# Kernel tuning notes

Measured on AMD Instinct MI355X. Metric: run time of the kernel, lower is better.

Reference implementation:

```python
import jax, jax.numpy as jnp
import numpy as np

B, C, S = 16, 8, 128
DT, DX, DY = 0.001, 1.0, 1.0
NUM_STEPS = 10
EPS = 1e-6


def _thomas(a, b, c, d):
    """Batched Thomas tridiagonal solve. a,b,c,d: [M,N] rows; solve along N."""
    aT, bT, cT, dT = a.T, b.T, c.T, d.T  # [N, M]
    zero = jnp.zeros_like(dT[0])

    def fwd(carry, inp):
        cs_p, ds_p = carry
        ai, bi, ci, di = inp
        denom = bi - ai * cs_p + EPS  # i=0: cs_p=0 -> denom = b0 + eps (matches torch)
        cs = ci / denom
        ds = (di - ai * ds_p) / denom
        return (cs, ds), (cs, ds)

    _, (c_star, d_star) = jax.lax.scan(fwd, (zero, zero), (aT, bT, cT, dT))

    def bwd(x_next, inp):
        ci, di = inp
        x = di - ci * x_next
        return x, x

    _, xs = jax.lax.scan(bwd, d_star[-1], (c_star[:-1], d_star[:-1]), reverse=True)
    x = jnp.concatenate([xs, d_star[-1:]], axis=0)  # [N, M]
    return x.T


def _diffuse_rows(u2d, coeff):
    """Implicit 1D diffusion along last axis. u2d, coeff: [M,N]."""
    a = -coeff
    c = -coeff
    b = 1.0 + 2.0 * coeff
    b = b.at[:, 0].set(1.0 + coeff[:, 0])
    b = b.at[:, -1].set(1.0 + coeff[:, -1])
    return _thomas(a, b, c, u2d)


def _forward(u, alpha_base, beta_base, alpha_time_coeff, beta_time_coeff, channel_mixing):
    Bb, Cc, H, W = u.shape
    half = DT / 2.0
    t = 0.0
    for _ in range(NUM_STEPS):
        # x half-step (coefficient alpha at time t)
        alpha = jnp.clip(alpha_base + alpha_time_coeff * t, EPS, 10.0)
        u = jnp.einsum('dc,bchw->bdhw', channel_mixing, u)
        uf = u.reshape(Bb * Cc, H, W)
        af = jnp.broadcast_to(alpha[None], (Bb, Cc, H, W)).reshape(Bb * Cc, H, W)
        uf = _diffuse_rows(uf.reshape(-1, W), af.reshape(-1, W) * half / DX**2).reshape(Bb * Cc, H, W)
        t += half
        # y full step (coefficient beta at time t+dt/2)
        beta = jnp.clip(beta_base + beta_time_coeff * t, EPS, 10.0)
        bf = jnp.broadcast_to(beta[None], (Bb, Cc, H, W)).reshape(Bb * Cc, H, W)
        ut = uf.transpose(0, 2, 1).reshape(-1, H)
        bt = bf.transpose(0, 2, 1).reshape(-1, H)
        ut = _diffuse_rows(ut, bt * DT / DY**2)
        uf = ut.reshape(Bb * Cc, W, H).transpose(0, 2, 1)
        t += half
        # x half-step (coefficient alpha at time t+dt)
        alpha = jnp.clip(alpha_base + alpha_time_coeff * t, EPS, 10.0)
        af = jnp.broadcast_to(alpha[None], (Bb, Cc, H, W)).reshape(Bb * Cc, H, W)
        uf = _diffuse_rows(uf.reshape(-1, W), af.reshape(-1, W) * half / DX**2).reshape(Bb * Cc, H, W)
        u = uf.reshape(Bb, Cc, H, W)
    return u


def setup_inputs() -> dict:
    key = jax.random.key(0)
    k_u, k_cm, k_atc, k_btc = jax.random.split(key, 4)
    u = jax.random.normal(k_u, (B, C, S, S), dtype=jnp.float32)
    alpha_base = jnp.ones((C, S, S), dtype=jnp.float32)
    beta_base = jnp.ones((C, S, S), dtype=jnp.float32)
    alpha_time_coeff = jax.random.normal(k_atc, (C, S, S), dtype=jnp.float32) * 0.01
    beta_time_coeff = jax.random.normal(k_btc, (C, S, S), dtype=jnp.float32) * 0.01
    channel_mixing = jnp.eye(C, dtype=jnp.float32) + jax.random.normal(k_cm, (C, C), dtype=jnp.float32) * 0.01
    return {
        'u': u,
        'alpha_base': alpha_base,
        'beta_base': beta_base,
        'alpha_time_coeff': alpha_time_coeff,
        'beta_time_coeff': beta_time_coeff,
        'channel_mixing': channel_mixing,
    }


def reference(u, alpha_base, beta_base, alpha_time_coeff, beta_time_coeff, channel_mixing):
    return _forward(u, alpha_base, beta_base, alpha_time_coeff, beta_time_coeff, channel_mixing)
```

## Files before the change

### kernel.cpp

```cpp
#include <hip/hip_runtime.h>
#include <hip/hip_fp16.h>


constexpr int S_  = 128;
constexpr int RS  = 129;
constexpr float EPSF = 1e-6f;
constexpr int CSS = 8 * 128 * 128;

__device__ __forceinline__ float2 decf(uint cb) {
    __half2 h = *reinterpret_cast<__half2*>(&cb);
    return __half22float2(h);
}

template <int N>
__device__ __forceinline__ void jrunN(const float (&e)[N], const float (&g)[N],
                                      float (&o)[N - 4]) {
    float x1[N];
    #pragma unroll
    for (int i = 1; i <= N - 2; ++i) x1[i] = fmaf(g[i], e[i - 1] + e[i + 1], e[i]);
    #pragma unroll
    for (int i = 2; i <= N - 3; ++i) o[i - 2] = fmaf(g[i], x1[i - 1] + x1[i + 1], e[i]);
}

__global__ __launch_bounds__(256) void coef_kernel(
    const float* __restrict__ ab, const float* __restrict__ atc,
    const float* __restrict__ bb, const float* __restrict__ btc,
    __half2* __restrict__ cf)
{
    for (int gc = blockIdx.x * 256 + threadIdx.x; gc < CSS; gc += gridDim.x * 256) {
        const int w = gc & 127, h = (gc >> 7) & 127;
        const float abv = ab[gc], atv = atc[gc], bbv = bb[gc], btv = btc[gc];
        const float nbY = (h == 0 || h == S_ - 1) ? 1.f : 2.f;
        const float nbX = (w == 0 || w == S_ - 1) ? 1.f : 2.f;
        for (int k = 0; k < 10; ++k) {
            const float ty = (2 * k + 1) * 0.0005f;
            const float tx = (2 * k + 2) * 0.0005f;
            float be = fminf(fmaxf(fmaf(btv, ty, bbv), EPSF), 10.f);
            float co = be * 0.001f;
            float rb = __builtin_amdgcn_rcpf(fmaf(nbY, co, 1.f) + EPSF);
            cf[k * CSS + gc] = __floats2half2_rn(rb * co, rb - 1.f);
            float al = fminf(fmaxf(fmaf(atv, tx, abv), EPSF), 10.f);
            co = al * 0.0005f;
            rb = __builtin_amdgcn_rcpf(fmaf(nbX, co, 1.f) + EPSF);
            cf[(10 + k) * CSS + gc] = __floats2half2_rn(rb * co, rb - 1.f);
        }
        float al = fminf(fmaxf(abv, EPSF), 10.f);
        float co = al * 0.0005f;
        float rb = __builtin_amdgcn_rcpf(fmaf(nbX, co, 1.f) + EPSF);
        cf[20 * CSS + gc] = __floats2half2_rn(rb * co, rb - 1.f);
    }
}

template <bool HEAD, bool LASTK>
__global__ __launch_bounds__(512, 2) void step_kernel(
    const void* __restrict__ usrc_, void* __restrict__ udst_,
    const __half2* __restrict__ cfy, const __half2* __restrict__ cfx,
    const __half2* __restrict__ cfx0, const float* __restrict__ cm)
{
    constexpr int POOL   = HEAD ? 288 * RS : 192 * RS;
    constexpr int OFF_A  = 0;
    constexpr int OFF_B  = 64 * RS;
    constexpr int OFF_CP = HEAD ? 192 * RS : 128 * RS;
    constexpr int OFF_X0 = 96 * RS;
    __shared__ float sP[POOL];
    const int tid = threadIdx.x;
    const int b   = blockIdx.x >> 4;
    const int h0  = (blockIdx.x & 15) << 3;

    if (HEAD) {
        const float* u0 = (const float*)usrc_;
        #pragma unroll
        for (int m = 0; m < 2; ++m) {
            const int col = tid + 512 * m;
            const int c = col >> 7, w = col & 127;
            #pragma unroll
            for (int hh = 0; hh < 12; ++hh) {
                const int gh = h0 - 2 + hh;
                float v = 0.f;
                if (gh >= 0 && gh < S_) v = u0[((b * 8 + c) * S_ + gh) * S_ + w];
                sP[(c * 12 + hh) * RS + w] = v;
            }
        }
        #pragma unroll
        for (int m = 0; m < 12; ++m) {
            const int task = tid + 512 * m;
            const int r = task >> 6, col2 = task & 63;
            const int c = r / 12, hh = r % 12;
            int gh = h0 - 2 + hh; gh = gh < 0 ? 0 : (gh >= S_ ? S_ - 1 : gh);
            const uint2 v = ((const uint2*)cfx0)[(c * S_ + gh) * 64 + col2];
            sP[OFF_CP + r * RS + col2 * 2]     = __uint_as_float(v.x);
            sP[OFF_CP + r * RS + col2 * 2 + 1] = __uint_as_float(v.y);
        }
        __syncthreads();
        {
            float M[64];
            #pragma unroll
            for (int i = 0; i < 64; ++i) M[i] = cm[i];
            #pragma unroll
            for (int m = 0; m < 3; ++m) {
                const int p = tid + 512 * m;
                const int hh = p >> 7, w = p & 127;
                float v[8], o[8];
                #pragma unroll
                for (int c = 0; c < 8; ++c) v[c] = sP[(c * 12 + hh) * RS + w];
                #pragma unroll
                for (int dd = 0; dd < 8; ++dd) {
                    float a = 0.f;
                    #pragma unroll
                    for (int c = 0; c < 8; ++c) a = fmaf(M[dd * 8 + c], v[c], a);
                    o[dd] = a;
                }
                #pragma unroll
                for (int c = 0; c < 8; ++c) sP[(c * 12 + hh) * RS + w] = o[c];
            }
        }
        __syncthreads();
        #pragma unroll
        for (int m = 0; m < 3; ++m) {
            const int task = tid + 512 * m;
            const int r96 = task % 96, wr = task / 96;
            const int c = r96 / 12, hh = r96 % 12;
            const int gh = h0 - 2 + hh;
            const bool rowin = (gh >= 0 && gh < S_);
            const int w0 = wr * 8;
            float e[12], g[12];
            #pragma unroll
            for (int j = 0; j < 12; ++j) {
                const int wj = w0 - 2 + j;
                const bool win = (wj >= 0 && wj < S_);
                const float dv = win ? sP[r96 * RS + wj] : 0.f;
                const uint cb = (rowin && win)
                    ? __float_as_uint(sP[OFF_CP + r96 * RS + wj]) : 0u;
                const float2 f = decf(cb);
                e[j] = (1.f + f.y) * dv;
                g[j] = f.x;
            }
            float o[8]; jrunN<12>(e, g, o);
            #pragma unroll
            for (int i = 0; i < 8; ++i) sP[OFF_X0 + r96 * RS + w0 + i] = o[i];
        }
        __syncthreads();
    }

    const __half* us = (const __half*)usrc_;
    #pragma unroll
    for (int m = 0; m < 2; ++m) {
        const int col = tid + 512 * m;
        const int c = col >> 7, w = col & 127;
        float e[12], g[12];
        #pragma unroll
        for (int hh = 0; hh < 12; ++hh) {
            const int gh = h0 - 2 + hh;
            const bool inr = (gh >= 0 && gh < S_);
            const int ghc = inr ? gh : 0;
            float dv;
            if (HEAD) dv = sP[OFF_X0 + (c * 12 + hh) * RS + w];
            else      dv = inr ? __half2float(us[((b * 8 + c) * S_ + ghc) * S_ + w]) : 0.f;
            const __half2 cy = cfy[(c * S_ + ghc) * S_ + w];
            const float2 f = __half22float2(cy);
            e[hh] = (1.f + f.y) * dv;
            g[hh] = inr ? f.x : 0.f;
        }
        float o[8]; jrunN<12>(e, g, o);
        #pragma unroll
        for (int i = 0; i < 8; ++i) sP[OFF_A + (c * 8 + i) * RS + w] = o[i];
    }
    #pragma unroll
    for (int m = 0; m < 8; ++m) {
        const int task = tid + 512 * m;
        const int r = task >> 6, col2 = task & 63;
        const int c = r >> 3, ho = r & 7;
        const uint2 v = ((const uint2*)cfx)[(c * S_ + h0 + ho) * 64 + col2];
        sP[OFF_CP + r * RS + col2 * 2]     = __uint_as_float(v.x);
        sP[OFF_CP + r * RS + col2 * 2 + 1] = __uint_as_float(v.y);
    }
    __syncthreads();

    float rbk[2][12], gk[2][12], xo[2][8];
    #pragma unroll
    for (int m = 0; m < 2; ++m) {
        const int run = tid + 512 * m;
        const int r = run & 63, wr = run >> 6;
        const int w0 = wr * 8;
        float e[12];
        #pragma unroll
        for (int j = 0; j < 12; ++j) {
            const int wj = w0 - 2 + j;
            const bool win = (wj >= 0 && wj < S_);
            const float dv = win ? sP[OFF_A + r * RS + wj] : 0.f;
            const uint cb = win ? __float_as_uint(sP[OFF_CP + r * RS + wj]) : 0u;
            const float2 f = decf(cb);
            rbk[m][j] = 1.f + f.y; gk[m][j] = f.x;
            e[j] = rbk[m][j] * dv;
        }
        jrunN<12>(e, gk[m], xo[m]);
    }

    if (LASTK) {
        float* ud = (float*)udst_;
        #pragma unroll
        for (int m = 0; m < 2; ++m) {
            const int run = tid + 512 * m;
            const int r = run & 63, wr = run >> 6;
            const int c = r >> 3, ho = r & 7;
            float4* dst4 = (float4*)&ud[((b * 8 + c) * S_ + h0 + ho) * S_ + wr * 8];
            dst4[0] = make_float4(xo[m][0], xo[m][1], xo[m][2], xo[m][3]);
            dst4[1] = make_float4(xo[m][4], xo[m][5], xo[m][6], xo[m][7]);
        }
    } else {
        #pragma unroll
        for (int m = 0; m < 2; ++m) {
            const int run = tid + 512 * m;
            const int r = run & 63, w0 = (run >> 6) * 8;
            #pragma unroll
            for (int i = 0; i < 8; ++i) sP[OFF_B + r * RS + w0 + i] = xo[m][i];
        }
        __syncthreads();
        float M[64];
        #pragma unroll
        for (int i = 0; i < 64; ++i) M[i] = cm[i];
        #pragma unroll
        for (int m = 0; m < 2; ++m) {
            const int p = tid + 512 * m;
            const int ho = p >> 7, w = p & 127;
            float v[8], o[8];
            #pragma unroll
            for (int c = 0; c < 8; ++c) v[c] = sP[OFF_B + (c * 8 + ho) * RS + w];
            #pragma unroll
            for (int dd = 0; dd < 8; ++dd) {
                float a = 0.f;
                #pragma unroll
                for (int c = 0; c < 8; ++c) a = fmaf(M[dd * 8 + c], v[c], a);
                o[dd] = a;
            }
            #pragma unroll
            for (int c = 0; c < 8; ++c) sP[OFF_A + (c * 8 + ho) * RS + w] = o[c];
        }
        __syncthreads();
        __half* ud = (__half*)udst_;
        #pragma unroll
        for (int m = 0; m < 2; ++m) {
            const int run = tid + 512 * m;
            const int r = run & 63, wr = run >> 6;
            const int w0 = wr * 8;
            const int c = r >> 3, ho = r & 7;
            float e[12];
            #pragma unroll
            for (int j = 0; j < 12; ++j) {
                const int wj = w0 - 2 + j;
                const bool win = (wj >= 0 && wj < S_);
                const float dv = win ? sP[OFF_A + r * RS + wj] : 0.f;
                e[j] = rbk[m][j] * dv;
            }
            float o[8]; jrunN<12>(e, gk[m], o);
            __half2* d2 = (__half2*)&ud[((b * 8 + c) * S_ + h0 + ho) * S_ + w0];
            d2[0] = __floats2half2_rn(o[0], o[1]);
            d2[1] = __floats2half2_rn(o[2], o[3]);
            d2[2] = __floats2half2_rn(o[4], o[5]);
            d2[3] = __floats2half2_rn(o[6], o[7]);
        }
    }
}

extern "C" void kernel_launch(void* const* d_in, const int* in_sizes, int n_in,
                              void* d_out, int out_size, void* d_ws, size_t ws_size,
                              hipStream_t stream) {
    const float* u_in = (const float*)d_in[0];
    const float* ab   = (const float*)d_in[1];
    const float* bbta = (const float*)d_in[2];
    const float* atc  = (const float*)d_in[3];
    const float* btc  = (const float*)d_in[4];
    const float* cm   = (const float*)d_in[5];
    float* uo = (float*)d_out;
    __half*  h1 = (__half*)d_ws;
    __half*  h2 = (__half*)((char*)d_ws + (8u << 20));
    __half2* cf = (__half2*)((char*)d_ws + (16u << 20));

    coef_kernel<<<dim3(512), dim3(256), 0, stream>>>(ab, atc, bbta, btc, cf);

    const dim3 g(256), blk(512);
    step_kernel<true, false><<<g, blk, 0, stream>>>(u_in, h1, cf + 0 * CSS,
                                                    cf + 10 * CSS, cf + 20 * CSS, cm);
    const __half* s = h1; __half* d = h2;
    for (int k = 1; k <= 8; ++k) {
        step_kernel<false, false><<<g, blk, 0, stream>>>(s, d, cf + k * CSS,
                                                         cf + (10 + k) * CSS, cf, cm);
        const __half* ns = d;
        d = (d == h2) ? h1 : h2;
        s = ns;
    }
    step_kernel<false, true><<<g, blk, 0, stream>>>(s, uo, cf + 9 * CSS,
                                                    cf + 19 * CSS, cf, cm);
}
```

Measured before the change: 166.5 us.

## Fuse all ten ADI steps into one persistent kernel with flag-synchronised halo exchange

Replaces the ten per-step kernel launches with one persistent kernel. Each block keeps its 8-row strip of all channels in LDS in fp32 across all steps. Only the two boundary rows on each side are exchanged with neighbouring blocks, through a double-buffered global halo array guarded by per-block progress flags. This removes launch overhead and the fp16 global round trip of the full field between steps. In exchange it needs all 256 blocks to be resident at once, uses relaxed atomics without explicit fences, and never resets the flags between calls, so repeated invocations could read stale halos.

```diff
diff --git a/kernel.cpp b/kernel.cpp
--- a/kernel.cpp
+++ b/kernel.cpp
@@ -5,12 +5,16 @@
 constexpr int S_  = 128;
 constexpr int RS  = 129;
 constexpr float EPSF = 1e-6f;
-constexpr int CSS = 8 * 128 * 128;
-
-__device__ __forceinline__ float2 decf(uint cb) {
-    __half2 h = *reinterpret_cast<__half2*>(&cb);
-    return __half22float2(h);
-}
+constexpr int CSS  = 8 * 128 * 128;
+constexpr int NBLK = 256;
+
+constexpr int OFF_U  = 0;
+constexpr int OFF_A  = 64 * RS;
+constexpr int OFF_B  = 128 * RS;
+constexpr int OFF_C  = 192 * RS;
+constexpr int OFF_ST = 64 * RS;
+constexpr int OFF_HB = 160 * RS;
+constexpr int POOL   = 256 * RS;
 
 template <int N>
 __device__ __forceinline__ void jrunN(const float (&e)[N], const float (&g)[N],
@@ -51,70 +55,56 @@
     }
 }
 
-template <bool HEAD, bool LASTK>
-__global__ __launch_bounds__(512, 2) void step_kernel(
-    const void* __restrict__ usrc_, void* __restrict__ udst_,
-    const __half2* __restrict__ cfy, const __half2* __restrict__ cfx,
-    const __half2* __restrict__ cfx0, const float* __restrict__ cm)
+__global__ __launch_bounds__(512, 2) void adi10_kernel(
+    const float* __restrict__ u0, float* __restrict__ uout,
+    const __half2* __restrict__ cf, const float* __restrict__ cm,
+    float* __restrict__ halo, unsigned* __restrict__ flags)
 {
-    constexpr int POOL   = HEAD ? 288 * RS : 192 * RS;
-    constexpr int OFF_A  = 0;
-    constexpr int OFF_B  = 64 * RS;
-    constexpr int OFF_CP = HEAD ? 192 * RS : 128 * RS;
-    constexpr int OFF_X0 = 96 * RS;
     __shared__ float sP[POOL];
-    const int tid = threadIdx.x;
-    const int b   = blockIdx.x >> 4;
-    const int h0  = (blockIdx.x & 15) << 3;
-
-    if (HEAD) {
-        const float* u0 = (const float*)usrc_;
-        #pragma unroll
-        for (int m = 0; m < 2; ++m) {
-            const int col = tid + 512 * m;
-            const int c = col >> 7, w = col & 127;
-            #pragma unroll
-            for (int hh = 0; hh < 12; ++hh) {
-                const int gh = h0 - 2 + hh;
-                float v = 0.f;
-                if (gh >= 0 && gh < S_) v = u0[((b * 8 + c) * S_ + gh) * S_ + w];
-                sP[(c * 12 + hh) * RS + w] = v;
-            }
-        }
-        #pragma unroll
-        for (int m = 0; m < 12; ++m) {
-            const int task = tid + 512 * m;
-            const int r = task >> 6, col2 = task & 63;
-            const int c = r / 12, hh = r % 12;
-            int gh = h0 - 2 + hh; gh = gh < 0 ? 0 : (gh >= S_ ? S_ - 1 : gh);
-            const uint2 v = ((const uint2*)cfx0)[(c * S_ + gh) * 64 + col2];
-            sP[OFF_CP + r * RS + col2 * 2]     = __uint_as_float(v.x);
-            sP[OFF_CP + r * RS + col2 * 2 + 1] = __uint_as_float(v.y);
-        }
-        __syncthreads();
-        {
-            float M[64];
-            #pragma unroll
-            for (int i = 0; i < 64; ++i) M[i] = cm[i];
-            #pragma unroll
-            for (int m = 0; m < 3; ++m) {
-                const int p = tid + 512 * m;
-                const int hh = p >> 7, w = p & 127;
-                float v[8], o[8];
-                #pragma unroll
-                for (int c = 0; c < 8; ++c) v[c] = sP[(c * 12 + hh) * RS + w];
-                #pragma unroll
-                for (int dd = 0; dd < 8; ++dd) {
-                    float a = 0.f;
-                    #pragma unroll
-                    for (int c = 0; c < 8; ++c) a = fmaf(M[dd * 8 + c], v[c], a);
-                    o[dd] = a;
-                }
-                #pragma unroll
-                for (int c = 0; c < 8; ++c) sP[(c * 12 + hh) * RS + w] = o[c];
-            }
-        }
-        __syncthreads();
+    const int tid   = threadIdx.x;
+    const int blk   = blockIdx.x;
+    const int b     = blk >> 4;
+    const int chunk = blk & 15;
+    const int h0    = chunk << 3;
+
+    #pragma unroll
+    for (int m = 0; m < 2; ++m) {
+        const int col = tid + 512 * m;
+        const int c = col >> 7, w = col & 127;
+        #pragma unroll
+        for (int hh = 0; hh < 12; ++hh) {
+            const int gh = h0 - 2 + hh;
+            float v = 0.f;
+            if (gh >= 0 && gh < S_) v = u0[((b * 8 + c) * S_ + gh) * S_ + w];
+            sP[OFF_ST + (c * 12 + hh) * RS + w] = v;
+        }
+    }
+    __syncthreads();
+    {
+        float M[64];
+        #pragma unroll
+        for (int i = 0; i < 64; ++i) M[i] = cm[i];
+        #pragma unroll
+        for (int m = 0; m < 3; ++m) {
+            const int p = tid + 512 * m;
+            const int hh = p >> 7, w = p & 127;
+            float v[8], o[8];
+            #pragma unroll
+            for (int c = 0; c < 8; ++c) v[c] = sP[OFF_ST + (c * 12 + hh) * RS + w];
+            #pragma unroll
+            for (int dd = 0; dd < 8; ++dd) {
+                float a = 0.f;
+                #pragma unroll
+                for (int c = 0; c < 8; ++c) a = fmaf(M[dd * 8 + c], v[c], a);
+                o[dd] = a;
+            }
+            #pragma unroll
+            for (int c = 0; c < 8; ++c) sP[OFF_ST + (c * 12 + hh) * RS + w] = o[c];
+        }
+    }
+    __syncthreads();
+    {
+        const __half2* cfx0 = cf + 20 * CSS;
         #pragma unroll
         for (int m = 0; m < 3; ++m) {
             const int task = tid + 512 * m;
@@ -122,142 +112,182 @@
             const int c = r96 / 12, hh = r96 % 12;
             const int gh = h0 - 2 + hh;
             const bool rowin = (gh >= 0 && gh < S_);
+            const int ghc = rowin ? gh : 0;
             const int w0 = wr * 8;
             float e[12], g[12];
             #pragma unroll
             for (int j = 0; j < 12; ++j) {
                 const int wj = w0 - 2 + j;
                 const bool win = (wj >= 0 && wj < S_);
-                const float dv = win ? sP[r96 * RS + wj] : 0.f;
-                const uint cb = (rowin && win)
-                    ? __float_as_uint(sP[OFF_CP + r96 * RS + wj]) : 0u;
-                const float2 f = decf(cb);
+                const float dv = win ? sP[OFF_ST + r96 * RS + wj] : 0.f;
+                float2 f = make_float2(0.f, 0.f);
+                if (rowin && win) f = __half22float2(cfx0[(c * S_ + ghc) * S_ + wj]);
                 e[j] = (1.f + f.y) * dv;
                 g[j] = f.x;
             }
             float o[8]; jrunN<12>(e, g, o);
-            #pragma unroll
-            for (int i = 0; i < 8; ++i) sP[OFF_X0 + r96 * RS + w0 + i] = o[i];
+            const int urow = (hh >= 2 && hh < 10)
+                ? OFF_U + (c * 8 + hh - 2) * RS
+                : OFF_HB + (c * 4 + (hh < 2 ? hh : hh - 8)) * RS;
+            #pragma unroll
+            for (int i = 0; i < 8; ++i) sP[urow + w0 + i] = o[i];
+        }
+    }
+    __syncthreads();
+
+    for (int k = 0; k < 10; ++k) {
+        const __half2* cfy  = cf + k * CSS;
+        const __half2* cfxk = cf + (10 + k) * CSS;
+
+        if (k > 0) {
+            if (tid == 0 && chunk > 0)
+                while (__hip_atomic_load(&flags[blk - 1], __ATOMIC_RELAXED,
+                                         __HIP_MEMORY_SCOPE_AGENT) < (unsigned)k)
+                    __builtin_amdgcn_s_sleep(2);
+            if (tid == 1 && chunk < 15)
+                while (__hip_atomic_load(&flags[blk + 1], __ATOMIC_RELAXED,
+                                         __HIP_MEMORY_SCOPE_AGENT) < (unsigned)k)
+                    __builtin_amdgcn_s_sleep(2);
+            __syncthreads();
+        }
+
+        const int rslot = (k - 1) & 1;
+        #pragma unroll
+        for (int m = 0; m < 2; ++m) {
+            const int col = tid + 512 * m;
+            const int c = col >> 7, w = col & 127;
+            float e[12], g[12];
+            #pragma unroll
+            for (int hh = 0; hh < 12; ++hh) {
+                const int gh = h0 - 2 + hh;
+                const bool inr = (gh >= 0 && gh < S_);
+                const int ghc = inr ? gh : 0;
+                float dv;
+                if (hh >= 2 && hh < 10) {
+                    dv = sP[OFF_U + (c * 8 + hh - 2) * RS + w];
+                } else if (k == 0) {
+                    dv = sP[OFF_HB + (c * 4 + (hh < 2 ? hh : hh - 8)) * RS + w];
+                } else if (!inr) {
+                    dv = 0.f;
+                } else {
+                    const int nb_ = (hh < 2) ? blk - 1 : blk + 1;
+                    const int e_  = (hh < 2) ? 2 + hh : hh - 10;
+                    dv = __hip_atomic_load(
+                        &halo[(rslot * NBLK + nb_) * 4096 + (e_ * 8 + c) * 128 + w],
+                        __ATOMIC_RELAXED, __HIP_MEMORY_SCOPE_AGENT);
+                }
+                const float2 f = __half22float2(cfy[(c * S_ + ghc) * S_ + w]);
+                e[hh] = (1.f + f.y) * dv;
+                g[hh] = inr ? f.x : 0.f;
+            }
+            float o[8]; jrunN<12>(e, g, o);
+            #pragma unroll
+            for (int i = 0; i < 8; ++i) sP[OFF_A + (c * 8 + i) * RS + w] = o[i];
+        }
+        #pragma unroll
+        for (int m = 0; m < 8; ++m) {
+            const int task = tid + 512 * m;
+            const int r = task >> 6, col2 = task & 63;
+            const int c = r >> 3, ho = r & 7;
+            const uint2 v = ((const uint2*)cfxk)[(c * S_ + h0 + ho) * 64 + col2];
+            sP[OFF_C + r * RS + col2 * 2]     = __uint_as_float(v.x);
+            sP[OFF_C + r * RS + col2 * 2 + 1] = __uint_as_float(v.y);
         }
         __syncthreads();
-    }
-
-    const __half* us = (const __half*)usrc_;
-    #pragma unroll
-    for (int m = 0; m < 2; ++m) {
-        const int col = tid + 512 * m;
-        const int c = col >> 7, w = col & 127;
-        float e[12], g[12];
-        #pragma unroll
-        for (int hh = 0; hh < 12; ++hh) {
-            const int gh = h0 - 2 + hh;
-            const bool inr = (gh >= 0 && gh < S_);
-            const int ghc = inr ? gh : 0;
-            float dv;
-            if (HEAD) dv = sP[OFF_X0 + (c * 12 + hh) * RS + w];
-            else      dv = inr ? __half2float(us[((b * 8 + c) * S_ + ghc) * S_ + w]) : 0.f;
-            const __half2 cy = cfy[(c * S_ + ghc) * S_ + w];
-            const float2 f = __half22float2(cy);
-            e[hh] = (1.f + f.y) * dv;
-            g[hh] = inr ? f.x : 0.f;
-        }
-        float o[8]; jrunN<12>(e, g, o);
-        #pragma unroll
-        for (int i = 0; i < 8; ++i) sP[OFF_A + (c * 8 + i) * RS + w] = o[i];
-    }
-    #pragma unroll
-    for (int m = 0; m < 8; ++m) {
-        const int task = tid + 512 * m;
-        const int r = task >> 6, col2 = task & 63;
-        const int c = r >> 3, ho = r & 7;
-        const uint2 v = ((const uint2*)cfx)[(c * S_ + h0 + ho) * 64 + col2];
-        sP[OFF_CP + r * RS + col2 * 2]     = __uint_as_float(v.x);
-        sP[OFF_CP + r * RS + col2 * 2 + 1] = __uint_as_float(v.y);
-    }
-    __syncthreads();
-
-    float rbk[2][12], gk[2][12], xo[2][8];
-    #pragma unroll
-    for (int m = 0; m < 2; ++m) {
-        const int run = tid + 512 * m;
-        const int r = run & 63, wr = run >> 6;
-        const int w0 = wr * 8;
-        float e[12];
-        #pragma unroll
-        for (int j = 0; j < 12; ++j) {
-            const int wj = w0 - 2 + j;
-            const bool win = (wj >= 0 && wj < S_);
-            const float dv = win ? sP[OFF_A + r * RS + wj] : 0.f;
-            const uint cb = win ? __float_as_uint(sP[OFF_CP + r * RS + wj]) : 0u;
-            const float2 f = decf(cb);
-            rbk[m][j] = 1.f + f.y; gk[m][j] = f.x;
-            e[j] = rbk[m][j] * dv;
-        }
-        jrunN<12>(e, gk[m], xo[m]);
-    }
-
-    if (LASTK) {
-        float* ud = (float*)udst_;
-        #pragma unroll
-        for (int m = 0; m < 2; ++m) {
-            const int run = tid + 512 * m;
-            const int r = run & 63, wr = run >> 6;
-            const int c = r >> 3, ho = r & 7;
-            float4* dst4 = (float4*)&ud[((b * 8 + c) * S_ + h0 + ho) * S_ + wr * 8];
-            dst4[0] = make_float4(xo[m][0], xo[m][1], xo[m][2], xo[m][3]);
-            dst4[1] = make_float4(xo[m][4], xo[m][5], xo[m][6], xo[m][7]);
-        }
-    } else {
-        #pragma unroll
-        for (int m = 0; m < 2; ++m) {
-            const int run = tid + 512 * m;
-            const int r = run & 63, w0 = (run >> 6) * 8;
-            #pragma unroll
-            for (int i = 0; i < 8; ++i) sP[OFF_B + r * RS + w0 + i] = xo[m][i];
-        }
-        __syncthreads();
-        float M[64];
-        #pragma unroll
-        for (int i = 0; i < 64; ++i) M[i] = cm[i];
-        #pragma unroll
-        for (int m = 0; m < 2; ++m) {
-            const int p = tid + 512 * m;
-            const int ho = p >> 7, w = p & 127;
-            float v[8], o[8];
-            #pragma unroll
-            for (int c = 0; c < 8; ++c) v[c] = sP[OFF_B + (c * 8 + ho) * RS + w];
-            #pragma unroll
-            for (int dd = 0; dd < 8; ++dd) {
-                float a = 0.f;
-                #pragma unroll
-                for (int c = 0; c < 8; ++c) a = fmaf(M[dd * 8 + c], v[c], a);
-                o[dd] = a;
-            }
-            #pragma unroll
-            for (int c = 0; c < 8; ++c) sP[OFF_A + (c * 8 + ho) * RS + w] = o[c];
-        }
-        __syncthreads();
-        __half* ud = (__half*)udst_;
+
+        float rbk[2][12], gk[2][12], xo[2][8];
         #pragma unroll
         for (int m = 0; m < 2; ++m) {
             const int run = tid + 512 * m;
             const int r = run & 63, wr = run >> 6;
             const int w0 = wr * 8;
-            const int c = r >> 3, ho = r & 7;
             float e[12];
             #pragma unroll
             for (int j = 0; j < 12; ++j) {
                 const int wj = w0 - 2 + j;
                 const bool win = (wj >= 0 && wj < S_);
                 const float dv = win ? sP[OFF_A + r * RS + wj] : 0.f;
+                uint cb = win ? __float_as_uint(sP[OFF_C + r * RS + wj]) : 0u;
+                const float2 f = __half22float2(*reinterpret_cast<__half2*>(&cb));
+                rbk[m][j] = 1.f + f.y; gk[m][j] = f.x;
                 e[j] = rbk[m][j] * dv;
             }
-            float o[8]; jrunN<12>(e, gk[m], o);
-            __half2* d2 = (__half2*)&ud[((b * 8 + c) * S_ + h0 + ho) * S_ + w0];
-            d2[0] = __floats2half2_rn(o[0], o[1]);
-            d2[1] = __floats2half2_rn(o[2], o[3]);
-            d2[2] = __floats2half2_rn(o[4], o[5]);
-            d2[3] = __floats2half2_rn(o[6], o[7]);
+            jrunN<12>(e, gk[m], xo[m]);
+        }
+
+        if (k == 9) {
+            #pragma unroll
+            for (int m = 0; m < 2; ++m) {
+                const int run = tid + 512 * m;
+                const int r = run & 63, wr = run >> 6;
+                const int c = r >> 3, ho = r & 7;
+                float4* dst4 = (float4*)&uout[((b * 8 + c) * S_ + h0 + ho) * S_ + wr * 8];
+                dst4[0] = make_float4(xo[m][0], xo[m][1], xo[m][2], xo[m][3]);
+                dst4[1] = make_float4(xo[m][4], xo[m][5], xo[m][6], xo[m][7]);
+            }
+        } else {
+            #pragma unroll
+            for (int m = 0; m < 2; ++m) {
+                const int run = tid + 512 * m;
+                const int r = run & 63, w0 = (run >> 6) * 8;
+                #pragma unroll
+                for (int i = 0; i < 8; ++i) sP[OFF_B + r * RS + w0 + i] = xo[m][i];
+            }
+            __syncthreads();
+            {
+                float M[64];
+                #pragma unroll
+                for (int i = 0; i < 64; ++i) M[i] = cm[i];
+                #pragma unroll
+                for (int m = 0; m < 2; ++m) {
+                    const int p = tid + 512 * m;
+                    const int ho = p >> 7, w = p & 127;
+                    float v[8], o[8];
+                    #pragma unroll
+                    for (int c = 0; c < 8; ++c) v[c] = sP[OFF_B + (c * 8 + ho) * RS + w];
+                    #pragma unroll
+                    for (int dd = 0; dd < 8; ++dd) {
+                        float a = 0.f;
+                        #pragma unroll
+                        for (int c = 0; c < 8; ++c) a = fmaf(M[dd * 8 + c], v[c], a);
+                        o[dd] = a;
+                    }
+                    #pragma unroll
+                    for (int c = 0; c < 8; ++c) sP[OFF_A + (c * 8 + ho) * RS + w] = o[c];
+                }
+            }
+            __syncthreads();
+            const int wslot = k & 1;
+            #pragma unroll
+            for (int m = 0; m < 2; ++m) {
+                const int run = tid + 512 * m;
+                const int r = run & 63, wr = run >> 6;
+                const int w0 = wr * 8;
+                const int c = r >> 3, ho = r & 7;
+                float e[12];
+                #pragma unroll
+                for (int j = 0; j < 12; ++j) {
+                    const int wj = w0 - 2 + j;
+                    const bool win = (wj >= 0 && wj < S_);
+                    const float dv = win ? sP[OFF_A + r * RS + wj] : 0.f;
+                    e[j] = rbk[m][j] * dv;
+                }
+                float o[8]; jrunN<12>(e, gk[m], o);
+                #pragma unroll
+                for (int i = 0; i < 8; ++i) sP[OFF_U + r * RS + w0 + i] = o[i];
+                if (ho < 2 || ho >= 6) {
+                    const int e_ = (ho < 2) ? ho : ho - 4;
+                    float* hp = &halo[(wslot * NBLK + blk) * 4096 + (e_ * 8 + c) * 128 + w0];
+                    #pragma unroll
+                    for (int i = 0; i < 8; ++i)
+                        __hip_atomic_store(&hp[i], o[i], __ATOMIC_RELAXED,
+                                           __HIP_MEMORY_SCOPE_AGENT);
+                }
+            }
+            __syncthreads();
+            if (tid == 0)
+                __hip_atomic_store(&flags[blk], (unsigned)(k + 1), __ATOMIC_RELAXED,
+                                   __HIP_MEMORY_SCOPE_AGENT);
         }
     }
 }
@@ -272,23 +302,11 @@
     const float* btc  = (const float*)d_in[4];
     const float* cm   = (const float*)d_in[5];
     float* uo = (float*)d_out;
-    __half*  h1 = (__half*)d_ws;
-    __half*  h2 = (__half*)((char*)d_ws + (8u << 20));
-    __half2* cf = (__half2*)((char*)d_ws + (16u << 20));
+
+    __half2*  cf    = (__half2*)d_ws;
+    float*    haloB = (float*)((char*)d_ws + (12u << 20));
+    unsigned* flags = (unsigned*)((char*)d_ws + (21u << 20));
 
     coef_kernel<<<dim3(512), dim3(256), 0, stream>>>(ab, atc, bbta, btc, cf);
-
-    const dim3 g(256), blk(512);
-    step_kernel<true, false><<<g, blk, 0, stream>>>(u_in, h1, cf + 0 * CSS,
-                                                    cf + 10 * CSS, cf + 20 * CSS, cm);
-    const __half* s = h1; __half* d = h2;
-    for (int k = 1; k <= 8; ++k) {
-        step_kernel<false, false><<<g, blk, 0, stream>>>(s, d, cf + k * CSS,
-                                                         cf + (10 + k) * CSS, cf, cm);
-        const __half* ns = d;
-        d = (d == h2) ? h1 : h2;
-        s = ns;
-    }
-    step_kernel<false, true><<<g, blk, 0, stream>>>(s, uo, cf + 9 * CSS,
-                                                    cf + 19 * CSS, cf, cm);
+    adi10_kernel<<<dim3(NBLK), dim3(512), 0, stream>>>(u_in, uo, cf, cm, haloB, flags);
 }
```

Result: slower. 247.8 us (+48.9%).

## Split head kernel and use XOR-swizzled shared layout with vectorized accesses

Applied to the files above, without the earlier changes.

Splits the templated step kernel into a dedicated head kernel and a steady-state step kernel. The steady-state kernel stores shared tiles in a 128-wide XOR-swizzled layout so threads can use float4 shared loads and stores without bank conflicts. It also loads two columns per thread as packed half2/uint2 from global memory and writes fp16 outputs as a single uint4. The aim is to cut shared-memory instruction count, bank conflicts and global transaction count in the nine repeated step launches. The exchange is more complex indexing and changed per-thread register pressure; launch bounds drop the min-blocks hint, which may change occupancy.

```diff
diff --git a/kernel.cpp b/kernel.cpp
--- a/kernel.cpp
+++ b/kernel.cpp
@@ -7,9 +7,13 @@
 constexpr float EPSF = 1e-6f;
 constexpr int CSS = 8 * 128 * 128;
 
-__device__ __forceinline__ float2 decf(uint cb) {
-    __half2 h = *reinterpret_cast<__half2*>(&cb);
-    return __half22float2(h);
+constexpr int SOFF_A = 0;
+constexpr int SOFF_B = 64 * 128;
+constexpr int SOFF_C = 128 * 128;
+constexpr int SPOOL  = 192 * 128;
+
+__device__ __forceinline__ int swad(int r, int b) {
+    return r * 128 + (((b) ^ (r & 31)) << 2);
 }
 
 template <int N>
@@ -51,45 +55,316 @@
     }
 }
 
-template <bool HEAD, bool LASTK>
-__global__ __launch_bounds__(512, 2) void step_kernel(
-    const void* __restrict__ usrc_, void* __restrict__ udst_,
+__global__ __launch_bounds__(512, 2) void head_kernel(
+    const float* __restrict__ u0, __half* __restrict__ ud,
     const __half2* __restrict__ cfy, const __half2* __restrict__ cfx,
     const __half2* __restrict__ cfx0, const float* __restrict__ cm)
 {
-    constexpr int POOL   = HEAD ? 288 * RS : 192 * RS;
+    constexpr int POOL   = 288 * RS;
     constexpr int OFF_A  = 0;
     constexpr int OFF_B  = 64 * RS;
-    constexpr int OFF_CP = HEAD ? 192 * RS : 128 * RS;
+    constexpr int OFF_CP = 192 * RS;
     constexpr int OFF_X0 = 96 * RS;
     __shared__ float sP[POOL];
     const int tid = threadIdx.x;
     const int b   = blockIdx.x >> 4;
     const int h0  = (blockIdx.x & 15) << 3;
 
-    if (HEAD) {
-        const float* u0 = (const float*)usrc_;
+    #pragma unroll
+    for (int m = 0; m < 2; ++m) {
+        const int col = tid + 512 * m;
+        const int c = col >> 7, w = col & 127;
+        #pragma unroll
+        for (int hh = 0; hh < 12; ++hh) {
+            const int gh = h0 - 2 + hh;
+            float v = 0.f;
+            if (gh >= 0 && gh < S_) v = u0[((b * 8 + c) * S_ + gh) * S_ + w];
+            sP[(c * 12 + hh) * RS + w] = v;
+        }
+    }
+    #pragma unroll
+    for (int m = 0; m < 12; ++m) {
+        const int task = tid + 512 * m;
+        const int r = task >> 6, col2 = task & 63;
+        const int c = r / 12, hh = r % 12;
+        int gh = h0 - 2 + hh; gh = gh < 0 ? 0 : (gh >= S_ ? S_ - 1 : gh);
+        const uint2 v = ((const uint2*)cfx0)[(c * S_ + gh) * 64 + col2];
+        sP[OFF_CP + r * RS + col2 * 2]     = __uint_as_float(v.x);
+        sP[OFF_CP + r * RS + col2 * 2 + 1] = __uint_as_float(v.y);
+    }
+    __syncthreads();
+    {
+        float M[64];
+        #pragma unroll
+        for (int i = 0; i < 64; ++i) M[i] = cm[i];
+        #pragma unroll
+        for (int m = 0; m < 3; ++m) {
+            const int p = tid + 512 * m;
+            const int hh = p >> 7, w = p & 127;
+            float v[8], o[8];
+            #pragma unroll
+            for (int c = 0; c < 8; ++c) v[c] = sP[(c * 12 + hh) * RS + w];
+            #pragma unroll
+            for (int dd = 0; dd < 8; ++dd) {
+                float a = 0.f;
+                #pragma unroll
+                for (int c = 0; c < 8; ++c) a = fmaf(M[dd * 8 + c], v[c], a);
+                o[dd] = a;
+            }
+            #pragma unroll
+            for (int c = 0; c < 8; ++c) sP[(c * 12 + hh) * RS + w] = o[c];
+        }
+    }
+    __syncthreads();
+    #pragma unroll
+    for (int m = 0; m < 3; ++m) {
+        const int task = tid + 512 * m;
+        const int r96 = task % 96, wr = task / 96;
+        const int hh = r96 % 12;
+        const int gh = h0 - 2 + hh;
+        const bool rowin = (gh >= 0 && gh < S_);
+        const int w0 = wr * 8;
+        float e[12], g[12];
+        #pragma unroll
+        for (int j = 0; j < 12; ++j) {
+            const int wj = w0 - 2 + j;
+            const bool win = (wj >= 0 && wj < S_);
+            const float dv = win ? sP[r96 * RS + wj] : 0.f;
+            uint cb = (rowin && win) ? __float_as_uint(sP[OFF_CP + r96 * RS + wj]) : 0u;
+            const float2 f = __half22float2(*reinterpret_cast<__half2*>(&cb));
+            e[j] = (1.f + f.y) * dv;
+            g[j] = f.x;
+        }
+        float o[8]; jrunN<12>(e, g, o);
+        #pragma unroll
+        for (int i = 0; i < 8; ++i) sP[OFF_X0 + r96 * RS + w0 + i] = o[i];
+    }
+    __syncthreads();
+
+    #pragma unroll
+    for (int m = 0; m < 2; ++m) {
+        const int col = tid + 512 * m;
+        const int c = col >> 7, w = col & 127;
+        float e[12], g[12];
+        #pragma unroll
+        for (int hh = 0; hh < 12; ++hh) {
+            const int gh = h0 - 2 + hh;
+            const bool inr = (gh >= 0 && gh < S_);
+            const int ghc = inr ? gh : 0;
+            const float dv = sP[OFF_X0 + (c * 12 + hh) * RS + w];
+            const float2 f = __half22float2(cfy[(c * S_ + ghc) * S_ + w]);
+            e[hh] = (1.f + f.y) * dv;
+            g[hh] = inr ? f.x : 0.f;
+        }
+        float o[8]; jrunN<12>(e, g, o);
+        #pragma unroll
+        for (int i = 0; i < 8; ++i) sP[OFF_A + (c * 8 + i) * RS + w] = o[i];
+    }
+    __syncthreads();
+    #pragma unroll
+    for (int m = 0; m < 8; ++m) {
+        const int task = tid + 512 * m;
+        const int r = task >> 6, col2 = task & 63;
+        const int c = r >> 3, ho = r & 7;
+        const uint2 v = ((const uint2*)cfx)[(c * S_ + h0 + ho) * 64 + col2];
+        sP[OFF_CP + r * RS + col2 * 2]     = __uint_as_float(v.x);
+        sP[OFF_CP + r * RS + col2 * 2 + 1] = __uint_as_float(v.y);
+    }
+    __syncthreads();
+
+    float rbk[2][12], gk[2][12], xo[2][8];
+    #pragma unroll
+    for (int m = 0; m < 2; ++m) {
+        const int run = tid + 512 * m;
+        const int r = run & 63, wr = run >> 6;
+        const int w0 = wr * 8;
+        float e[12];
+        #pragma unroll
+        for (int j = 0; j < 12; ++j) {
+            const int wj = w0 - 2 + j;
+            const bool win = (wj >= 0 && wj < S_);
+            const float dv = win ? sP[OFF_A + r * RS + wj] : 0.f;
+            uint cb = win ? __float_as_uint(sP[OFF_CP + r * RS + wj]) : 0u;
+            const float2 f = __half22float2(*reinterpret_cast<__half2*>(&cb));
+            rbk[m][j] = 1.f + f.y; gk[m][j] = f.x;
+            e[j] = rbk[m][j] * dv;
+        }
+        jrunN<12>(e, gk[m], xo[m]);
+    }
+    #pragma unroll
+    for (int m = 0; m < 2; ++m) {
+        const int run = tid + 512 * m;
+        const int r = run & 63, w0 = (run >> 6) * 8;
+        #pragma unroll
+        for (int i = 0; i < 8; ++i) sP[OFF_B + r * RS + w0 + i] = xo[m][i];
+    }
+    __syncthreads();
+    {
+        float M[64];
+        #pragma unroll
+        for (int i = 0; i < 64; ++i) M[i] = cm[i];
         #pragma unroll
         for (int m = 0; m < 2; ++m) {
-            const int col = tid + 512 * m;
-            const int c = col >> 7, w = col & 127;
+            const int p = tid + 512 * m;
+            const int ho = p >> 7, w = p & 127;
+            float v[8], o[8];
+            #pragma unroll
+            for (int c = 0; c < 8; ++c) v[c] = sP[OFF_B + (c * 8 + ho) * RS + w];
+            #pragma unroll
+            for (int dd = 0; dd < 8; ++dd) {
+                float a = 0.f;
+                #pragma unroll
+                for (int c = 0; c < 8; ++c) a = fmaf(M[dd * 8 + c], v[c], a);
+                o[dd] = a;
+            }
+            #pragma unroll
+            for (int c = 0; c < 8; ++c) sP[OFF_A + (c * 8 + ho) * RS + w] = o[c];
+        }
+    }
+    __syncthreads();
+    #pragma unroll
+    for (int m = 0; m < 2; ++m) {
+        const int run = tid + 512 * m;
+        const int r = run & 63, wr = run >> 6;
+        const int w0 = wr * 8;
+        const int c = r >> 3, ho = r & 7;
+        float e[12];
+        #pragma unroll
+        for (int j = 0; j < 12; ++j) {
+            const int wj = w0 - 2 + j;
+            const bool win = (wj >= 0 && wj < S_);
+            const float dv = win ? sP[OFF_A + r * RS + wj] : 0.f;
+            e[j] = rbk[m][j] * dv;
+        }
+        float o[8]; jrunN<12>(e, gk[m], o);
+        __half2* d2 = (__half2*)&ud[((b * 8 + c) * S_ + h0 + ho) * S_ + w0];
+        d2[0] = __floats2half2_rn(o[0], o[1]);
+        d2[1] = __floats2half2_rn(o[2], o[3]);
+        d2[2] = __floats2half2_rn(o[4], o[5]);
+        d2[3] = __floats2half2_rn(o[6], o[7]);
+    }
+}
+
+template <bool LASTK>
+__global__ __launch_bounds__(512) void stepS_kernel(
+    const __half* __restrict__ us, void* __restrict__ udst_,
+    const __half2* __restrict__ cfy, const __half2* __restrict__ cfx,
+    const float* __restrict__ cm)
+{
+    __shared__ __align__(16) float sP[SPOOL];
+    const int tid = threadIdx.x;
+    const int b   = blockIdx.x >> 4;
+    const int h0  = (blockIdx.x & 15) << 3;
+
+    {
+        const int c  = tid >> 6;
+        const int wp = tid & 63;
+        const int wbase = 2 * wp;
+        uint du[12]; uint2 dc[12];
+        #pragma unroll
+        for (int hh = 0; hh < 12; ++hh) {
+            const int gh = h0 - 2 + hh;
+            const bool inr = (gh >= 0 && gh < S_);
+            const int ghc = inr ? gh : 0;
+            du[hh] = inr ? *(const uint*)&us[((b * 8 + c) * S_ + ghc) * S_ + wbase] : 0u;
+            dc[hh] = *(const uint2*)&cfy[(c * S_ + ghc) * S_ + wbase];
+        }
+        float o2[2][8];
+        #pragma unroll
+        for (int s = 0; s < 2; ++s) {
+            float e[12], g[12];
             #pragma unroll
             for (int hh = 0; hh < 12; ++hh) {
                 const int gh = h0 - 2 + hh;
-                float v = 0.f;
-                if (gh >= 0 && gh < S_) v = u0[((b * 8 + c) * S_ + gh) * S_ + w];
-                sP[(c * 12 + hh) * RS + w] = v;
-            }
-        }
-        #pragma unroll
-        for (int m = 0; m < 12; ++m) {
+                const bool inr = (gh >= 0 && gh < S_);
+                uint ub = du[hh];
+                __half2 hu = *reinterpret_cast<__half2*>(&ub);
+                const float dv = s ? __high2float(hu) : __low2float(hu);
+                uint cb = s ? dc[hh].y : dc[hh].x;
+                const float2 f = __half22float2(*reinterpret_cast<__half2*>(&cb));
+                e[hh] = (1.f + f.y) * dv;
+                g[hh] = inr ? f.x : 0.f;
+            }
+            jrunN<12>(e, g, o2[s]);
+        }
+        #pragma unroll
+        for (int i = 0; i < 8; ++i) {
+            const int r = c * 8 + i;
+            float2* p = (float2*)&sP[SOFF_A + r * 128 +
+                                     (((wp >> 1) ^ (r & 31)) << 2) + 2 * (wp & 1)];
+            *p = make_float2(o2[0][i], o2[1][i]);
+        }
+    }
+    {
+        const uint* cfxu = (const uint*)cfx;
+        #pragma unroll
+        for (int m = 0; m < 4; ++m) {
             const int task = tid + 512 * m;
-            const int r = task >> 6, col2 = task & 63;
-            const int c = r / 12, hh = r % 12;
-            int gh = h0 - 2 + hh; gh = gh < 0 ? 0 : (gh >= S_ ? S_ - 1 : gh);
-            const uint2 v = ((const uint2*)cfx0)[(c * S_ + gh) * 64 + col2];
-            sP[OFF_CP + r * RS + col2 * 2]     = __uint_as_float(v.x);
-            sP[OFF_CP + r * RS + col2 * 2 + 1] = __uint_as_float(v.y);
+            const int r = task >> 5, col4 = task & 31;
+            const int c = r >> 3, ho = r & 7;
+            const uint4 v = *(const uint4*)&cfxu[(c * S_ + h0 + ho) * S_ + col4 * 4];
+            *(float4*)&sP[SOFF_C + swad(r, col4)] =
+                make_float4(__uint_as_float(v.x), __uint_as_float(v.y),
+                            __uint_as_float(v.z), __uint_as_float(v.w));
+        }
+    }
+    __syncthreads();
+
+    float rbk[2][12], gk[2][12], xo[2][8];
+    #pragma unroll
+    for (int m = 0; m < 2; ++m) {
+        const int r  = tid & 63;
+        const int wr = (tid >> 6) + 8 * m;
+        const int w0 = wr * 8;
+        float f[16]; uint cb[16];
+        #pragma unroll
+        for (int i = 0; i < 4; ++i) {
+            const int bb = (w0 >> 2) - 1 + i;
+            if (bb >= 0 && bb < 32) {
+                const float4 va = *(const float4*)&sP[SOFF_A + swad(r, bb)];
+                const float4 vc = *(const float4*)&sP[SOFF_C + swad(r, bb)];
+                f[4 * i + 0] = va.x; f[4 * i + 1] = va.y;
+                f[4 * i + 2] = va.z; f[4 * i + 3] = va.w;
+                cb[4 * i + 0] = __float_as_uint(vc.x);
+                cb[4 * i + 1] = __float_as_uint(vc.y);
+                cb[4 * i + 2] = __float_as_uint(vc.z);
+                cb[4 * i + 3] = __float_as_uint(vc.w);
+            } else {
+                f[4 * i + 0] = f[4 * i + 1] = f[4 * i + 2] = f[4 * i + 3] = 0.f;
+                cb[4 * i + 0] = cb[4 * i + 1] = cb[4 * i + 2] = cb[4 * i + 3] = 0u;
+            }
+        }
+        float e[12];
+        #pragma unroll
+        for (int j = 0; j < 12; ++j) {
+            uint c_ = cb[j + 2];
+            const float2 fc = __half22float2(*reinterpret_cast<__half2*>(&c_));
+            rbk[m][j] = 1.f + fc.y; gk[m][j] = fc.x;
+            e[j] = rbk[m][j] * f[j + 2];
+        }
+        jrunN<12>(e, gk[m], xo[m]);
+    }
+
+    if (LASTK) {
+        float* ud = (float*)udst_;
+        #pragma unroll
+        for (int m = 0; m < 2; ++m) {
+            const int r  = tid & 63;
+            const int wr = (tid >> 6) + 8 * m;
+            const int c = r >> 3, ho = r & 7;
+            float4* dst4 = (float4*)&ud[((b * 8 + c) * S_ + h0 + ho) * S_ + wr * 8];
+            dst4[0] = make_float4(xo[m][0], xo[m][1], xo[m][2], xo[m][3]);
+            dst4[1] = make_float4(xo[m][4], xo[m][5], xo[m][6], xo[m][7]);
+        }
+    } else {
+        #pragma unroll
+        for (int m = 0; m < 2; ++m) {
+            const int r  = tid & 63;
+            const int wr = (tid >> 6) + 8 * m;
+            *(float4*)&sP[SOFF_B + swad(r, 2 * wr)] =
+                make_float4(xo[m][0], xo[m][1], xo[m][2], xo[m][3]);
+            *(float4*)&sP[SOFF_B + swad(r, 2 * wr + 1)] =
+                make_float4(xo[m][4], xo[m][5], xo[m][6], xo[m][7]);
         }
         __syncthreads();
         {
@@ -97,12 +372,15 @@
             #pragma unroll
             for (int i = 0; i < 64; ++i) M[i] = cm[i];
             #pragma unroll
-            for (int m = 0; m < 3; ++m) {
+            for (int m = 0; m < 2; ++m) {
                 const int p = tid + 512 * m;
-                const int hh = p >> 7, w = p & 127;
+                const int ho = p >> 7, w = p & 127;
                 float v[8], o[8];
                 #pragma unroll
-                for (int c = 0; c < 8; ++c) v[c] = sP[(c * 12 + hh) * RS + w];
+                for (int c = 0; c < 8; ++c) {
+                    const int r = c * 8 + ho;
+                    v[c] = sP[SOFF_B + r * 128 + (((w >> 2) ^ (r & 31)) << 2) + (w & 3)];
+                }
                 #pragma unroll
                 for (int dd = 0; dd < 8; ++dd) {
                     float a = 0.f;
@@ -111,153 +389,46 @@
                     o[dd] = a;
                 }
                 #pragma unroll
-                for (int c = 0; c < 8; ++c) sP[(c * 12 + hh) * RS + w] = o[c];
-            }
-        }
-        __syncthreads();
-        #pragma unroll
-        for (int m = 0; m < 3; ++m) {
-            const int task = tid + 512 * m;
-            const int r96 = task % 96, wr = task / 96;
-            const int c = r96 / 12, hh = r96 % 12;
-            const int gh = h0 - 2 + hh;
-            const bool rowin = (gh >= 0 && gh < S_);
-            const int w0 = wr * 8;
-            float e[12], g[12];
-            #pragma unroll
-            for (int j = 0; j < 12; ++j) {
-                const int wj = w0 - 2 + j;
-                const bool win = (wj >= 0 && wj < S_);
-                const float dv = win ? sP[r96 * RS + wj] : 0.f;
-                const uint cb = (rowin && win)
-                    ? __float_as_uint(sP[OFF_CP + r96 * RS + wj]) : 0u;
-                const float2 f = decf(cb);
-                e[j] = (1.f + f.y) * dv;
-                g[j] = f.x;
-            }
-            float o[8]; jrunN<12>(e, g, o);
-            #pragma unroll
-            for (int i = 0; i < 8; ++i) sP[OFF_X0 + r96 * RS + w0 + i] = o[i];
-        }
-        __syncthreads();
-    }
-
-    const __half* us = (const __half*)usrc_;
-    #pragma unroll
-    for (int m = 0; m < 2; ++m) {
-        const int col = tid + 512 * m;
-        const int c = col >> 7, w = col & 127;
-        float e[12], g[12];
-        #pragma unroll
-        for (int hh = 0; hh < 12; ++hh) {
-            const int gh = h0 - 2 + hh;
-            const bool inr = (gh >= 0 && gh < S_);
-            const int ghc = inr ? gh : 0;
-            float dv;
-            if (HEAD) dv = sP[OFF_X0 + (c * 12 + hh) * RS + w];
-            else      dv = inr ? __half2float(us[((b * 8 + c) * S_ + ghc) * S_ + w]) : 0.f;
-            const __half2 cy = cfy[(c * S_ + ghc) * S_ + w];
-            const float2 f = __half22float2(cy);
-            e[hh] = (1.f + f.y) * dv;
-            g[hh] = inr ? f.x : 0.f;
-        }
-        float o[8]; jrunN<12>(e, g, o);
-        #pragma unroll
-        for (int i = 0; i < 8; ++i) sP[OFF_A + (c * 8 + i) * RS + w] = o[i];
-    }
-    #pragma unroll
-    for (int m = 0; m < 8; ++m) {
-        const int task = tid + 512 * m;
-        const int r = task >> 6, col2 = task & 63;
-        const int c = r >> 3, ho = r & 7;
-        const uint2 v = ((const uint2*)cfx)[(c * S_ + h0 + ho) * 64 + col2];
-        sP[OFF_CP + r * RS + col2 * 2]     = __uint_as_float(v.x);
-        sP[OFF_CP + r * RS + col2 * 2 + 1] = __uint_as_float(v.y);
-    }
-    __syncthreads();
-
-    float rbk[2][12], gk[2][12], xo[2][8];
-    #pragma unroll
-    for (int m = 0; m < 2; ++m) {
-        const int run = tid + 512 * m;
-        const int r = run & 63, wr = run >> 6;
-        const int w0 = wr * 8;
-        float e[12];
-        #pragma unroll
-        for (int j = 0; j < 12; ++j) {
-            const int wj = w0 - 2 + j;
-            const bool win = (wj >= 0 && wj < S_);
-            const float dv = win ? sP[OFF_A + r * RS + wj] : 0.f;
-            const uint cb = win ? __float_as_uint(sP[OFF_CP + r * RS + wj]) : 0u;
-            const float2 f = decf(cb);
-            rbk[m][j] = 1.f + f.y; gk[m][j] = f.x;
-            e[j] = rbk[m][j] * dv;
-        }
-        jrunN<12>(e, gk[m], xo[m]);
-    }
-
-    if (LASTK) {
-        float* ud = (float*)udst_;
-        #pragma unroll
-        for (int m = 0; m < 2; ++m) {
-            const int run = tid + 512 * m;
-            const int r = run & 63, wr = run >> 6;
-            const int c = r >> 3, ho = r & 7;
-            float4* dst4 = (float4*)&ud[((b * 8 + c) * S_ + h0 + ho) * S_ + wr * 8];
-            dst4[0] = make_float4(xo[m][0], xo[m][1], xo[m][2], xo[m][3]);
-            dst4[1] = make_float4(xo[m][4], xo[m][5], xo[m][6], xo[m][7]);
-        }
-    } else {
-        #pragma unroll
-        for (int m = 0; m < 2; ++m) {
-            const int run = tid + 512 * m;
-            const int r = run & 63, w0 = (run >> 6) * 8;
-            #pragma unroll
-            for (int i = 0; i < 8; ++i) sP[OFF_B + r * RS + w0 + i] = xo[m][i];
-        }
-        __syncthreads();
-        float M[64];
-        #pragma unroll
-        for (int i = 0; i < 64; ++i) M[i] = cm[i];
-        #pragma unroll
-        for (int m = 0; m < 2; ++m) {
-            const int p = tid + 512 * m;
-            const int ho = p >> 7, w = p & 127;
-            float v[8], o[8];
-            #pragma unroll
-            for (int c = 0; c < 8; ++c) v[c] = sP[OFF_B + (c * 8 + ho) * RS + w];
-            #pragma unroll
-            for (int dd = 0; dd < 8; ++dd) {
-                float a = 0.f;
-                #pragma unroll
-                for (int c = 0; c < 8; ++c) a = fmaf(M[dd * 8 + c], v[c], a);
-                o[dd] = a;
-            }
-            #pragma unroll
-            for (int c = 0; c < 8; ++c) sP[OFF_A + (c * 8 + ho) * RS + w] = o[c];
+                for (int c = 0; c < 8; ++c) {
+                    const int r = c * 8 + ho;
+                    sP[SOFF_A + r * 128 + (((w >> 2) ^ (r & 31)) << 2) + (w & 3)] = o[c];
+                }
+            }
         }
         __syncthreads();
         __half* ud = (__half*)udst_;
         #pragma unroll
         for (int m = 0; m < 2; ++m) {
-            const int run = tid + 512 * m;
-            const int r = run & 63, wr = run >> 6;
+            const int r  = tid & 63;
+            const int wr = (tid >> 6) + 8 * m;
             const int w0 = wr * 8;
             const int c = r >> 3, ho = r & 7;
+            float f[16];
+            #pragma unroll
+            for (int i = 0; i < 4; ++i) {
+                const int bb = (w0 >> 2) - 1 + i;
+                if (bb >= 0 && bb < 32) {
+                    const float4 va = *(const float4*)&sP[SOFF_A + swad(r, bb)];
+                    f[4 * i + 0] = va.x; f[4 * i + 1] = va.y;
+                    f[4 * i + 2] = va.z; f[4 * i + 3] = va.w;
+                } else {
+                    f[4 * i + 0] = f[4 * i + 1] = f[4 * i + 2] = f[4 * i + 3] = 0.f;
+                }
+            }
             float e[12];
             #pragma unroll
-            for (int j = 0; j < 12; ++j) {
-                const int wj = w0 - 2 + j;
-                const bool win = (wj >= 0 && wj < S_);
-                const float dv = win ? sP[OFF_A + r * RS + wj] : 0.f;
-                e[j] = rbk[m][j] * dv;
-            }
+            for (int j = 0; j < 12; ++j) e[j] = rbk[m][j] * f[j + 2];
             float o[8]; jrunN<12>(e, gk[m], o);
-            __half2* d2 = (__half2*)&ud[((b * 8 + c) * S_ + h0 + ho) * S_ + w0];
-            d2[0] = __floats2half2_rn(o[0], o[1]);
-            d2[1] = __floats2half2_rn(o[2], o[3]);
-            d2[2] = __floats2half2_rn(o[4], o[5]);
-            d2[3] = __floats2half2_rn(o[6], o[7]);
+            __half2 q0 = __floats2half2_rn(o[0], o[1]);
+            __half2 q1 = __floats2half2_rn(o[2], o[3]);
+            __half2 q2 = __floats2half2_rn(o[4], o[5]);
+            __half2 q3 = __floats2half2_rn(o[6], o[7]);
+            uint4 pk;
+            pk.x = *reinterpret_cast<uint*>(&q0);
+            pk.y = *reinterpret_cast<uint*>(&q1);
+            pk.z = *reinterpret_cast<uint*>(&q2);
+            pk.w = *reinterpret_cast<uint*>(&q3);
+            *(uint4*)&ud[((b * 8 + c) * S_ + h0 + ho) * S_ + w0] = pk;
         }
     }
 }
@@ -279,16 +450,16 @@
     coef_kernel<<<dim3(512), dim3(256), 0, stream>>>(ab, atc, bbta, btc, cf);
 
     const dim3 g(256), blk(512);
-    step_kernel<true, false><<<g, blk, 0, stream>>>(u_in, h1, cf + 0 * CSS,
-                                                    cf + 10 * CSS, cf + 20 * CSS, cm);
+    head_kernel<<<g, blk, 0, stream>>>(u_in, h1, cf + 0 * CSS, cf + 10 * CSS,
+                                       cf + 20 * CSS, cm);
     const __half* s = h1; __half* d = h2;
     for (int k = 1; k <= 8; ++k) {
-        step_kernel<false, false><<<g, blk, 0, stream>>>(s, d, cf + k * CSS,
-                                                         cf + (10 + k) * CSS, cf, cm);
+        stepS_kernel<false><<<g, blk, 0, stream>>>(s, d, cf + k * CSS,
+                                                   cf + (10 + k) * CSS, cm);
         const __half* ns = d;
         d = (d == h2) ? h1 : h2;
         s = ns;
     }
-    step_kernel<false, true><<<g, blk, 0, stream>>>(s, uo, cf + 9 * CSS,
-                                                    cf + 19 * CSS, cf, cm);
-}
+    stepS_kernel<true><<<g, blk, 0, stream>>>(s, uo, cf + 9 * CSS,
+                                              cf + 19 * CSS, cm);
+}
```

Measured after the change: 152.7 us. -8.3%, faster.
